# Kernel tuning notes

Hardware: AMD Instinct MI355X
Metric: run time of the kernel (lower is better)

The kernel has to match this reference:

```python
import jax, jax.numpy as jnp
import numpy as np

TOP_K = 32
OBS_RADIUS = 1.0
N = 4096
IN_DIM = 4


def setup_inputs() -> dict:
    key = jax.random.key(0)
    ks = jax.random.split(key, 10)
    s = 0.05
    return {
        "states": jax.random.normal(ks[0], (N, 4), jnp.float32),
        "goals": jax.random.normal(ks[1], (N, 2), jnp.float32),
        "W1": jax.random.normal(ks[2], (64, IN_DIM + 1), jnp.float32) * s,
        "b1": jnp.zeros((64,), jnp.float32),
        "W2": jax.random.normal(ks[3], (128, 64), jnp.float32) * s,
        "b2": jnp.zeros((128,), jnp.float32),
        "Wd1": jax.random.normal(ks[4], (64, 132), jnp.float32) * s,
        "bd1": jnp.zeros((64,), jnp.float32),
        "Wd2": jax.random.normal(ks[5], (128, 64), jnp.float32) * s,
        "bd2": jnp.zeros((128,), jnp.float32),
        "Wd3": jax.random.normal(ks[6], (64, 128), jnp.float32) * s,
        "bd3": jnp.zeros((64,), jnp.float32),
        "Wd4": jax.random.normal(ks[7], (4, 64), jnp.float32) * s,
        "bd4": jnp.zeros((4,), jnp.float32),
    }


def reference(states, goals, W1, b1, W2, b2, Wd1, bd1, Wd2, bd2, Wd3, bd3, Wd4, bd4):
    n = states.shape[0]
    dt = states.dtype
    # pairwise relative states + one-hot self indicator -> [N, N, 5]
    x = states[:, None, :] - states[None, :, :]
    x = jnp.concatenate([x, jnp.eye(n, dtype=dt)[:, :, None]], axis=2)
    # remove_distant_agents: keep TOP_K nearest neighbors by planar distance
    d = jnp.sqrt(jnp.sum(x[:, :, :2] ** 2, axis=2) + 1e-4)  # [N, N]
    _, idx = jax.lax.top_k(-d, TOP_K)                        # [N, K]
    xk = jnp.take_along_axis(x, idx[:, :, None], axis=1)     # [N, K, 5]
    # observation-radius mask (torch reshape [N,K,1]->[N,1,K] == transpose here)
    dist = jnp.linalg.norm(xk[:, :, :2], axis=2)             # [N, K]
    mask = (dist < OBS_RADIUS).astype(dt).reshape(n, 1, TOP_K)
    # NOTE: original uses a raw reshape [N,K,5]->[N,5,K] (not a transpose); match it
    h = xk.reshape(n, IN_DIM + 1, TOP_K)
    # pointwise (kernel-1) conv stack 5 -> 64 -> 128
    h = jax.nn.relu(jnp.einsum('oc,ncp->nop', W1, h) + b1[None, :, None])
    h = jax.nn.relu(jnp.einsum('oc,ncp->nop', W2, h) + b2[None, :, None])
    # original does torch.max(...)[1]: ARGMAX indices, promoted to float by cat
    x_local = jnp.argmax(h * mask, axis=2).astype(dt)        # [N, 128]
    rel = states[:, :2] - goals
    feat = jnp.concatenate([x_local, rel, states[:, 2:]], axis=1)  # [N, 132]
    z = jax.nn.relu(feat @ Wd1.T + bd1)
    z = jax.nn.relu(z @ Wd2.T + bd2)
    z = jax.nn.relu(z @ Wd3.T + bd3)
    z = z @ Wd4.T + bd4
    k = 2.0 * jax.nn.sigmoid(z) + 0.2                        # [N, 4] gains
    state = jnp.concatenate([rel, states[:, 2:]], axis=1)    # [N, 4]
    a_x = -(k[:, 0] * state[:, 0] + k[:, 1] * state[:, 2])
    a_y = -(k[:, 2] * state[:, 1] + k[:, 3] * state[:, 3])
    return jnp.stack([a_x, a_y], axis=1)                     # [N, 2]
```

## Files before the change

### kernel.cpp

```cpp
#include <hip/hip_runtime.h>
#include <math.h>

#define NAGENT 4096
#define TOPK 32
#define AGB 4
#define DAGB 16
#define CANDCAP 2048

__global__ __launch_bounds__(256) void topk_kernel(
    const float* __restrict__ states, int* __restrict__ idx_out)
{
    const int i = blockIdx.x;
    const int t = threadIdx.x;
    __shared__ unsigned int hist[1024];
    __shared__ unsigned int ps[256];
    __shared__ unsigned int ps2[32];
    __shared__ unsigned long long cand[CANDCAP];
    __shared__ int ccount;
    __shared__ unsigned int cutB;

    #pragma unroll
    for (int u = 0; u < 4; ++u) hist[t + u * 256] = 0u;
    if (t == 0) ccount = 0;

    const float4 si = ((const float4*)states)[i];
    __syncthreads();

    unsigned int mybits[16];
    #pragma unroll
    for (int u = 0; u < 16; ++u) {
        int j = t + u * 256;
        float4 sj = ((const float4*)states)[j];
        float dx = __fsub_rn(si.x, sj.x);
        float dy = __fsub_rn(si.y, sj.y);
        float s  = __fadd_rn(__fadd_rn(__fmul_rn(dx, dx), __fmul_rn(dy, dy)), 1e-4f);
        unsigned int b = __float_as_uint(sqrtf(s));
        mybits[u] = b;
        atomicAdd(&hist[b >> 21], 1u);
    }
    __syncthreads();

    ps[t] = hist[t * 4 + 0] + hist[t * 4 + 1] + hist[t * 4 + 2] + hist[t * 4 + 3];
    __syncthreads();
    if (t < 32) {
        unsigned int s = 0;
        #pragma unroll
        for (int q = 0; q < 8; ++q) s += ps[t * 8 + q];
        ps2[t] = s;
    }
    __syncthreads();

    if (t == 0) {
        unsigned int cum = 0;
        int g2 = 0;
        while (cum + ps2[g2] < TOPK) { cum += ps2[g2]; ++g2; }
        int g1 = g2 * 8;
        while (cum + ps[g1] < TOPK) { cum += ps[g1]; ++g1; }
        int b = g1 * 4;
        for (;;) { cum += hist[b]; if (cum >= TOPK) break; ++b; }
        cutB = (unsigned int)b;
    }
    __syncthreads();

    const unsigned int B = cutB;
    #pragma unroll
    for (int u = 0; u < 16; ++u) {
        if ((mybits[u] >> 21) <= B) {
            int pos = atomicAdd(&ccount, 1);
            if (pos < CANDCAP)
                cand[pos] = ((unsigned long long)mybits[u] << 32)
                          | (unsigned int)(t + u * 256);
        }
    }
    __syncthreads();

    const int C = (ccount < CANDCAP) ? ccount : CANDCAP;
    for (int q = t; q < C; q += 256) {
        unsigned long long key = cand[q];
        int rank = 0;
        for (int r = 0; r < C; ++r) rank += (cand[r] < key) ? 1 : 0;
        if (rank < TOPK) idx_out[i * TOPK + rank] = (int)(key & 0xffffffffu);
    }
}

__global__ __launch_bounds__(256) void feat_kernel(
    const float* __restrict__ states, const float* __restrict__ goals,
    const float* __restrict__ W1, const float* __restrict__ b1,
    const float* __restrict__ W2, const float* __restrict__ b2,
    const int* __restrict__ idx_in, float* __restrict__ feat_ws)
{
    const int t = threadIdx.x;
    const int a = t >> 6;
    const int l = t & 63;
    const int i = blockIdx.x * AGB + a;

    __shared__ __attribute__((aligned(16))) float w2a[64 * 68];
    __shared__ __attribute__((aligned(16))) float w2b[64 * 68];
    __shared__ __attribute__((aligned(16))) float w1s[320];
    __shared__ __attribute__((aligned(16))) float b1s[64];
    __shared__ __attribute__((aligned(16))) float b2s[128];
    __shared__ __attribute__((aligned(16))) float flat[AGB][160];
    __shared__ __attribute__((aligned(16))) float maskv[AGB][32];
    __shared__ __attribute__((aligned(16))) float h1[AGB][2048];

    #pragma unroll
    for (int u = 0; u < 32; ++u) {
        int e = t + u * 256;
        int o = e >> 6, c = e & 63;
        float v = W2[e];
        int dst = c * 68 + ((o >> 3) << 2) + (o & 3);
        if (o & 4) w2b[dst] = v; else w2a[dst] = v;
    }
    for (int e = t; e < 320; e += 256) w1s[e] = W1[e];
    if (t < 64)  b1s[t] = b1[t];
    if (t < 128) b2s[t] = b2[t];

    if (l < 32) {
        int j = idx_in[i * TOPK + l];
        float4 sj  = ((const float4*)states)[j];
        float4 siv = ((const float4*)states)[i];
        float d0 = siv.x - sj.x;
        float d1 = siv.y - sj.y;
        float d2 = siv.z - sj.z;
        float d3 = siv.w - sj.w;
        flat[a][l * 5 + 0] = d0;
        flat[a][l * 5 + 1] = d1;
        flat[a][l * 5 + 2] = d2;
        flat[a][l * 5 + 3] = d3;
        flat[a][l * 5 + 4] = (j == i) ? 1.0f : 0.0f;
        float dist = sqrtf(__fadd_rn(__fmul_rn(d0, d0), __fmul_rn(d1, d1)));
        maskv[a][l] = (dist < 1.0f) ? 1.0f : 0.0f;
    } else if (l < 36) {
        int f = l - 32;
        float4 siv = ((const float4*)states)[i];
        float2 gi  = ((const float2*)goals)[i];
        float v = (f == 0) ? (siv.x - gi.x)
                : (f == 1) ? (siv.y - gi.y)
                : (f == 2) ? siv.z : siv.w;
        feat_ws[i * 132 + 128 + f] = v;
    }
    __syncthreads();

    #pragma unroll
    for (int u = 0; u < 32; ++u) {
        int e = u * 64 + l;
        int p = e & 31, o1 = e >> 5;
        float acc = b1s[o1];
        #pragma unroll
        for (int f = 0; f < 5; ++f)
            acc += w1s[o1 * 5 + f] * flat[a][f * 32 + p];
        h1[a][o1 * 32 + p] = fmaxf(acc, 0.0f);
    }
    __syncthreads();

    const int ow = l & 15;
    const int pt = l >> 4;
    float acc[8][8];
    #pragma unroll
    for (int k = 0; k < 8; ++k)
        #pragma unroll
        for (int q = 0; q < 8; ++q) acc[k][q] = 0.0f;

    for (int c = 0; c < 64; ++c) {
        float4 wA = *(const float4*)&w2a[c * 68 + ow * 4];
        float4 wB = *(const float4*)&w2b[c * 68 + ow * 4];
        float4 hA = *(const float4*)&h1[a][c * 32 + pt * 8];
        float4 hB = *(const float4*)&h1[a][c * 32 + pt * 8 + 4];
        float wv[8] = {wA.x, wA.y, wA.z, wA.w, wB.x, wB.y, wB.z, wB.w};
        float hv[8] = {hA.x, hA.y, hA.z, hA.w, hB.x, hB.y, hB.z, hB.w};
        #pragma unroll
        for (int k = 0; k < 8; ++k)
            #pragma unroll
            for (int q = 0; q < 8; ++q)
                acc[k][q] += wv[k] * hv[q];
    }

    float4 mA = *(const float4*)&maskv[a][pt * 8];
    float4 mB = *(const float4*)&maskv[a][pt * 8 + 4];
    float mv[8] = {mA.x, mA.y, mA.z, mA.w, mB.x, mB.y, mB.z, mB.w};
    #pragma unroll
    for (int k = 0; k < 8; ++k) {
        float bb = b2s[ow * 8 + k];
        unsigned long long best = 0ull;
        #pragma unroll
        for (int q = 0; q < 8; ++q) {
            float val = fmaxf(acc[k][q] + bb, 0.0f) * mv[q];
            unsigned long long key =
                ((unsigned long long)__float_as_uint(val) << 32)
                | (unsigned int)(31 - (pt * 8 + q));
            if (key > best) best = key;
        }
        unsigned long long o1 = __shfl_xor(best, 16, 64); if (o1 > best) best = o1;
        unsigned long long o2 = __shfl_xor(best, 32, 64); if (o2 > best) best = o2;
        if (pt == 0) {
            int pbest = 31 - (int)(best & 63ull);
            feat_ws[i * 132 + ow * 8 + k] = (float)pbest;
        }
    }
}

__global__ __launch_bounds__(256) void dense_kernel(
    const float* __restrict__ feat_ws,
    const float* __restrict__ Wd1, const float* __restrict__ bd1,
    const float* __restrict__ Wd2, const float* __restrict__ bd2,
    const float* __restrict__ Wd3, const float* __restrict__ bd3,
    const float* __restrict__ Wd4, const float* __restrict__ bd4,
    float* __restrict__ out)
{
    const int t = threadIdx.x;
    const int w = t >> 6;
    const int l = t & 63;
    const int A0 = blockIdx.x * DAGB;

    __shared__ float wd1s[64 * 133];
    __shared__ float wd2s[128 * 65];
    __shared__ float wd3s[64 * 129];
    __shared__ float wd4s[4 * 65];
    __shared__ float bd1s[64], bd2s[128], bd3s[64], bd4s[4];
    __shared__ __attribute__((aligned(16))) float fl[DAGB * 132];
    __shared__ __attribute__((aligned(16))) float z1[DAGB][64];
    __shared__ __attribute__((aligned(16))) float z2[DAGB][128];
    __shared__ __attribute__((aligned(16))) float z3[DAGB][64];
    __shared__ float kvs[DAGB][4];

    for (int e = t; e < 8448; e += 256) wd1s[(e / 132) * 133 + (e % 132)] = Wd1[e];
    for (int e = t; e < 8192; e += 256) wd2s[(e >> 6) * 65 + (e & 63)]   = Wd2[e];
    for (int e = t; e < 8192; e += 256) wd3s[(e >> 7) * 129 + (e & 127)] = Wd3[e];
    if (t < 256) wd4s[(t >> 6) * 65 + (t & 63)] = Wd4[t];
    if (t < 64)  bd1s[t] = bd1[t];
    if (t < 128) bd2s[t] = bd2[t];
    if (t < 64)  bd3s[t] = bd3[t];
    if (t < 4)   bd4s[t] = bd4[t];
    for (int e = t; e < DAGB * 132; e += 256) fl[e] = feat_ws[A0 * 132 + e];
    __syncthreads();

    const int gbase = w * 4;

    {
        float a0 = bd1s[l], a1 = bd1s[l], a2 = bd1s[l], a3 = bd1s[l];
        for (int k = 0; k < 33; ++k) {
            float w0 = wd1s[l * 133 + 4 * k + 0];
            float w1v = wd1s[l * 133 + 4 * k + 1];
            float w2v = wd1s[l * 133 + 4 * k + 2];
            float w3 = wd1s[l * 133 + 4 * k + 3];
            float4 f0 = *(const float4*)&fl[(gbase + 0) * 132 + 4 * k];
            float4 f1 = *(const float4*)&fl[(gbase + 1) * 132 + 4 * k];
            float4 f2 = *(const float4*)&fl[(gbase + 2) * 132 + 4 * k];
            float4 f3 = *(const float4*)&fl[(gbase + 3) * 132 + 4 * k];
            a0 += w0 * f0.x; a0 += w1v * f0.y; a0 += w2v * f0.z; a0 += w3 * f0.w;
            a1 += w0 * f1.x; a1 += w1v * f1.y; a1 += w2v * f1.z; a1 += w3 * f1.w;
            a2 += w0 * f2.x; a2 += w1v * f2.y; a2 += w2v * f2.z; a2 += w3 * f2.w;
            a3 += w0 * f3.x; a3 += w1v * f3.y; a3 += w2v * f3.z; a3 += w3 * f3.w;
        }
        z1[gbase + 0][l] = fmaxf(a0, 0.0f);
        z1[gbase + 1][l] = fmaxf(a1, 0.0f);
        z1[gbase + 2][l] = fmaxf(a2, 0.0f);
        z1[gbase + 3][l] = fmaxf(a3, 0.0f);
    }

    {
        float accA[4], accB[4];
        #pragma unroll
        for (int g = 0; g < 4; ++g) { accA[g] = bd2s[l]; accB[g] = bd2s[l + 64]; }
        for (int k = 0; k < 16; ++k) {
            float wa0 = wd2s[l * 65 + 4 * k + 0], wa1 = wd2s[l * 65 + 4 * k + 1];
            float wa2 = wd2s[l * 65 + 4 * k + 2], wa3 = wd2s[l * 65 + 4 * k + 3];
            float wb0 = wd2s[(l + 64) * 65 + 4 * k + 0], wb1 = wd2s[(l + 64) * 65 + 4 * k + 1];
            float wb2 = wd2s[(l + 64) * 65 + 4 * k + 2], wb3 = wd2s[(l + 64) * 65 + 4 * k + 3];
            #pragma unroll
            for (int g = 0; g < 4; ++g) {
                float4 f = *(const float4*)&z1[gbase + g][4 * k];
                accA[g] += wa0 * f.x; accA[g] += wa1 * f.y;
                accA[g] += wa2 * f.z; accA[g] += wa3 * f.w;
                accB[g] += wb0 * f.x; accB[g] += wb1 * f.y;
                accB[g] += wb2 * f.z; accB[g] += wb3 * f.w;
            }
        }
        #pragma unroll
        for (int g = 0; g < 4; ++g) {
            z2[gbase + g][l]      = fmaxf(accA[g], 0.0f);
            z2[gbase + g][l + 64] = fmaxf(accB[g], 0.0f);
        }
    }

    {
        float acc[4];
        #pragma unroll
        for (int g = 0; g < 4; ++g) acc[g] = bd3s[l];
        for (int k = 0; k < 32; ++k) {
            float w0 = wd3s[l * 129 + 4 * k + 0], w1v = wd3s[l * 129 + 4 * k + 1];
            float w2v = wd3s[l * 129 + 4 * k + 2], w3 = wd3s[l * 129 + 4 * k + 3];
            #pragma unroll
            for (int g = 0; g < 4; ++g) {
                float4 f = *(const float4*)&z2[gbase + g][4 * k];
                acc[g] += w0 * f.x; acc[g] += w1v * f.y;
                acc[g] += w2v * f.z; acc[g] += w3 * f.w;
            }
        }
        #pragma unroll
        for (int g = 0; g < 4; ++g) z3[gbase + g][l] = fmaxf(acc[g], 0.0f);
    }

    if (l < 16) {
        int g = l >> 2, o = l & 3;
        float acc = bd4s[o];
        for (int c = 0; c < 64; ++c) acc += wd4s[o * 65 + c] * z3[gbase + g][c];
        kvs[gbase + g][o] = 2.0f / (1.0f + expf(-acc)) + 0.2f;
    }
    __syncthreads();

    if (l < 8) {
        int g = l >> 1, axis = l & 1;
        float ka = kvs[gbase + g][2 * axis + 0];
        float kb = kvs[gbase + g][2 * axis + 1];
        float rel = fl[(gbase + g) * 132 + 128 + axis];
        float vel = fl[(gbase + g) * 132 + 130 + axis];
        out[(A0 + gbase + g) * 2 + axis] = -(ka * rel + kb * vel);
    }
}

extern "C" void kernel_launch(void* const* d_in, const int* in_sizes, int n_in,
                              void* d_out, int out_size, void* d_ws, size_t ws_size,
                              hipStream_t stream)
{
    const float* states = (const float*)d_in[0];
    const float* goals  = (const float*)d_in[1];
    const float* W1  = (const float*)d_in[2];
    const float* b1  = (const float*)d_in[3];
    const float* W2  = (const float*)d_in[4];
    const float* b2  = (const float*)d_in[5];
    const float* Wd1 = (const float*)d_in[6];
    const float* bd1 = (const float*)d_in[7];
    const float* Wd2 = (const float*)d_in[8];
    const float* bd2 = (const float*)d_in[9];
    const float* Wd3 = (const float*)d_in[10];
    const float* bd3 = (const float*)d_in[11];
    const float* Wd4 = (const float*)d_in[12];
    const float* bd4 = (const float*)d_in[13];

    const size_t idx_bytes = (size_t)NAGENT * TOPK * 4;
    int*   idx     = (int*)d_ws;
    float* feat_ws = (float*)((char*)d_ws + idx_bytes);
    float* out     = (float*)d_out;

    topk_kernel<<<NAGENT, 256, 0, stream>>>(states, idx);
    feat_kernel<<<NAGENT / AGB, 256, 0, stream>>>(states, goals, W1, b1, W2, b2,
                                                  idx, feat_ws);
    dense_kernel<<<NAGENT / DAGB, 256, 0, stream>>>(feat_ws, Wd1, bd1, Wd2, bd2,
                                                    Wd3, bd3, Wd4, bd4, out);
}
```

Baseline: 155.6 us.

## Use linear distance histogram bins in top-k and read dense weights from global

The top-k histogram now bins distances linearly (distance*256, clamped to 1023) rather than by the top float bits, so the cutoff bin sits at a finer granularity and fewer candidates reach the quadratic rank sort. The dense kernel stops staging all MLP weights into shared memory and loads them directly from global memory as float4 vectors, which removes a large per-block copy and cuts LDS usage, allowing higher occupancy. The trade-off is that weight reads now depend on L1/L2 cache hits. The linear binning also relies on distances mostly falling below 4.

```diff
diff --git a/kernel.cpp b/kernel.cpp
--- a/kernel.cpp
+++ b/kernel.cpp
@@ -34,9 +34,11 @@
         float dx = __fsub_rn(si.x, sj.x);
         float dy = __fsub_rn(si.y, sj.y);
         float s  = __fadd_rn(__fadd_rn(__fmul_rn(dx, dx), __fmul_rn(dy, dy)), 1e-4f);
-        unsigned int b = __float_as_uint(sqrtf(s));
-        mybits[u] = b;
-        atomicAdd(&hist[b >> 21], 1u);
+        float dv = sqrtf(s);
+        mybits[u] = __float_as_uint(dv);
+        unsigned int bin = (unsigned int)(dv * 256.0f);
+        if (bin > 1023u) bin = 1023u;
+        atomicAdd(&hist[bin], 1u);
     }
     __syncthreads();
 
@@ -65,7 +67,10 @@
     const unsigned int B = cutB;
     #pragma unroll
     for (int u = 0; u < 16; ++u) {
-        if ((mybits[u] >> 21) <= B) {
+        float dv = __uint_as_float(mybits[u]);
+        unsigned int bin = (unsigned int)(dv * 256.0f);
+        if (bin > 1023u) bin = 1023u;
+        if (bin <= B) {
             int pos = atomicAdd(&ccount, 1);
             if (pos < CANDCAP)
                 cand[pos] = ((unsigned long long)mybits[u] << 32)
@@ -212,45 +217,30 @@
     const int l = t & 63;
     const int A0 = blockIdx.x * DAGB;
 
-    __shared__ float wd1s[64 * 133];
-    __shared__ float wd2s[128 * 65];
-    __shared__ float wd3s[64 * 129];
-    __shared__ float wd4s[4 * 65];
-    __shared__ float bd1s[64], bd2s[128], bd3s[64], bd4s[4];
     __shared__ __attribute__((aligned(16))) float fl[DAGB * 132];
     __shared__ __attribute__((aligned(16))) float z1[DAGB][64];
     __shared__ __attribute__((aligned(16))) float z2[DAGB][128];
     __shared__ __attribute__((aligned(16))) float z3[DAGB][64];
     __shared__ float kvs[DAGB][4];
 
-    for (int e = t; e < 8448; e += 256) wd1s[(e / 132) * 133 + (e % 132)] = Wd1[e];
-    for (int e = t; e < 8192; e += 256) wd2s[(e >> 6) * 65 + (e & 63)]   = Wd2[e];
-    for (int e = t; e < 8192; e += 256) wd3s[(e >> 7) * 129 + (e & 127)] = Wd3[e];
-    if (t < 256) wd4s[(t >> 6) * 65 + (t & 63)] = Wd4[t];
-    if (t < 64)  bd1s[t] = bd1[t];
-    if (t < 128) bd2s[t] = bd2[t];
-    if (t < 64)  bd3s[t] = bd3[t];
-    if (t < 4)   bd4s[t] = bd4[t];
     for (int e = t; e < DAGB * 132; e += 256) fl[e] = feat_ws[A0 * 132 + e];
     __syncthreads();
 
     const int gbase = w * 4;
 
     {
-        float a0 = bd1s[l], a1 = bd1s[l], a2 = bd1s[l], a3 = bd1s[l];
+        float bb = bd1[l];
+        float a0 = bb, a1 = bb, a2 = bb, a3 = bb;
         for (int k = 0; k < 33; ++k) {
-            float w0 = wd1s[l * 133 + 4 * k + 0];
-            float w1v = wd1s[l * 133 + 4 * k + 1];
-            float w2v = wd1s[l * 133 + 4 * k + 2];
-            float w3 = wd1s[l * 133 + 4 * k + 3];
+            float4 wv = *(const float4*)&Wd1[l * 132 + 4 * k];
             float4 f0 = *(const float4*)&fl[(gbase + 0) * 132 + 4 * k];
             float4 f1 = *(const float4*)&fl[(gbase + 1) * 132 + 4 * k];
             float4 f2 = *(const float4*)&fl[(gbase + 2) * 132 + 4 * k];
             float4 f3 = *(const float4*)&fl[(gbase + 3) * 132 + 4 * k];
-            a0 += w0 * f0.x; a0 += w1v * f0.y; a0 += w2v * f0.z; a0 += w3 * f0.w;
-            a1 += w0 * f1.x; a1 += w1v * f1.y; a1 += w2v * f1.z; a1 += w3 * f1.w;
-            a2 += w0 * f2.x; a2 += w1v * f2.y; a2 += w2v * f2.z; a2 += w3 * f2.w;
-            a3 += w0 * f3.x; a3 += w1v * f3.y; a3 += w2v * f3.z; a3 += w3 * f3.w;
+            a0 += wv.x * f0.x; a0 += wv.y * f0.y; a0 += wv.z * f0.z; a0 += wv.w * f0.w;
+            a1 += wv.x * f1.x; a1 += wv.y * f1.y; a1 += wv.z * f1.z; a1 += wv.w * f1.w;
+            a2 += wv.x * f2.x; a2 += wv.y * f2.y; a2 += wv.z * f2.z; a2 += wv.w * f2.w;
+            a3 += wv.x * f3.x; a3 += wv.y * f3.y; a3 += wv.z * f3.z; a3 += wv.w * f3.w;
         }
         z1[gbase + 0][l] = fmaxf(a0, 0.0f);
         z1[gbase + 1][l] = fmaxf(a1, 0.0f);
@@ -260,20 +250,19 @@
 
     {
         float accA[4], accB[4];
-        #pragma unroll
-        for (int g = 0; g < 4; ++g) { accA[g] = bd2s[l]; accB[g] = bd2s[l + 64]; }
+        float bA = bd2[l], bB = bd2[l + 64];
+        #pragma unroll
+        for (int g = 0; g < 4; ++g) { accA[g] = bA; accB[g] = bB; }
         for (int k = 0; k < 16; ++k) {
-            float wa0 = wd2s[l * 65 + 4 * k + 0], wa1 = wd2s[l * 65 + 4 * k + 1];
-            float wa2 = wd2s[l * 65 + 4 * k + 2], wa3 = wd2s[l * 65 + 4 * k + 3];
-            float wb0 = wd2s[(l + 64) * 65 + 4 * k + 0], wb1 = wd2s[(l + 64) * 65 + 4 * k + 1];
-            float wb2 = wd2s[(l + 64) * 65 + 4 * k + 2], wb3 = wd2s[(l + 64) * 65 + 4 * k + 3];
+            float4 wa = *(const float4*)&Wd2[l * 64 + 4 * k];
+            float4 wb = *(const float4*)&Wd2[(l + 64) * 64 + 4 * k];
             #pragma unroll
             for (int g = 0; g < 4; ++g) {
                 float4 f = *(const float4*)&z1[gbase + g][4 * k];
-                accA[g] += wa0 * f.x; accA[g] += wa1 * f.y;
-                accA[g] += wa2 * f.z; accA[g] += wa3 * f.w;
-                accB[g] += wb0 * f.x; accB[g] += wb1 * f.y;
-                accB[g] += wb2 * f.z; accB[g] += wb3 * f.w;
+                accA[g] += wa.x * f.x; accA[g] += wa.y * f.y;
+                accA[g] += wa.z * f.z; accA[g] += wa.w * f.w;
+                accB[g] += wb.x * f.x; accB[g] += wb.y * f.y;
+                accB[g] += wb.z * f.z; accB[g] += wb.w * f.w;
             }
         }
         #pragma unroll
@@ -285,16 +274,16 @@
 
     {
         float acc[4];
-        #pragma unroll
-        for (int g = 0; g < 4; ++g) acc[g] = bd3s[l];
+        float bb = bd3[l];
+        #pragma unroll
+        for (int g = 0; g < 4; ++g) acc[g] = bb;
         for (int k = 0; k < 32; ++k) {
-            float w0 = wd3s[l * 129 + 4 * k + 0], w1v = wd3s[l * 129 + 4 * k + 1];
-            float w2v = wd3s[l * 129 + 4 * k + 2], w3 = wd3s[l * 129 + 4 * k + 3];
+            float4 wv = *(const float4*)&Wd3[l * 128 + 4 * k];
             #pragma unroll
             for (int g = 0; g < 4; ++g) {
                 float4 f = *(const float4*)&z2[gbase + g][4 * k];
-                acc[g] += w0 * f.x; acc[g] += w1v * f.y;
-                acc[g] += w2v * f.z; acc[g] += w3 * f.w;
+                acc[g] += wv.x * f.x; acc[g] += wv.y * f.y;
+                acc[g] += wv.z * f.z; acc[g] += wv.w * f.w;
             }
         }
         #pragma unroll
@@ -303,8 +292,8 @@
 
     if (l < 16) {
         int g = l >> 2, o = l & 3;
-        float acc = bd4s[o];
-        for (int c = 0; c < 64; ++c) acc += wd4s[o * 65 + c] * z3[gbase + g][c];
+        float acc = bd4[o];
+        for (int c = 0; c < 64; ++c) acc += Wd4[o * 64 + c] * z3[gbase + g][c];
         kvs[gbase + g][o] = 2.0f / (1.0f + expf(-acc)) + 0.2f;
     }
     __syncthreads();
```

Result: faster. 152.5 us (-2.0%).
